# Kernel optimization log

Measured on AMD Instinct MI355X. Metric: run time of the kernel, lower is better.

Reference implementation:

```python
import jax, jax.numpy as jnp
import numpy as np

N = 100000        # nodes
E = 1600000       # edges
D = 32            # hidden dim
C = 2             # num classes
NL = 4            # layer_num - 1 GIN layers
G = 512           # graphs in batch
BN_EPS = 1e-3     # keras BatchNormalization default epsilon


def setup_inputs() -> dict:
    key = jax.random.key(0)
    ks = jax.random.split(key, 16)
    s = 0.1
    return {
        "node_embeddings": jax.random.normal(ks[0], (N, D), dtype=jnp.float32),
        "edge_index": jax.random.randint(ks[1], (2, E), 0, N, dtype=jnp.int32),
        "batch": jnp.sort(jax.random.randint(ks[2], (N,), 0, G, dtype=jnp.int32)),
        # MLP inner dense + BN (per GIN layer)
        "W1": jax.random.normal(ks[3], (NL, D, D), dtype=jnp.float32) * s,
        "b1": jnp.zeros((NL, D), jnp.float32),
        "bn1_g": jnp.ones((NL, D), jnp.float32),
        "bn1_b": jnp.zeros((NL, D), jnp.float32),
        # MLP output dense
        "W2": jax.random.normal(ks[4], (NL, D, D), dtype=jnp.float32) * s,
        "b2": jnp.zeros((NL, D), jnp.float32),
        # ApplyNodeFunc BN
        "bn2_g": jnp.ones((NL, D), jnp.float32),
        "bn2_b": jnp.zeros((NL, D), jnp.float32),
        # outer per-layer BN
        "norm_g": jnp.ones((NL, D), jnp.float32),
        "norm_b": jnp.zeros((NL, D), jnp.float32),
        # readout heads: one Dense(num_classes) per hidden_rep level (layer_num of them)
        "dense_W": jax.random.normal(ks[5], (NL + 1, D, C), dtype=jnp.float32) * s,
        "dense_b": jnp.zeros((NL + 1, C), jnp.float32),
    }


def _bn(x, g, b):
    # inference-mode BatchNorm with init moving stats (mean=0, var=1)
    return x * (g / jnp.sqrt(1.0 + BN_EPS)) + b


def reference(node_embeddings, edge_index, batch, W1, b1, bn1_g, bn1_b,
              W2, b2, bn2_g, bn2_b, norm_g, norm_b, dense_W, dense_b):
    src, dst = edge_index[0], edge_index[1]
    h = node_embeddings
    hidden = [h]
    for i in range(NL):
        # GIN aggregation: (1+eps)*h + sum of neighbor features (eps=0)
        agg = jax.ops.segment_sum(h[src], dst, num_segments=N)  # [N, D]
        z = h + agg
        # ApplyNodeFunc: MLP (Dense->BN->ReLU->Dense) then BN + ReLU
        z = jax.nn.relu(_bn(z @ W1[i] + b1[i], bn1_g[i], bn1_b[i]))
        z = z @ W2[i] + b2[i]
        z = jax.nn.relu(_bn(z, bn2_g[i], bn2_b[i]))
        # outer norm + relu
        h = jax.nn.relu(_bn(z, norm_g[i], norm_b[i]))
        hidden.append(h)
    # readout: segment-sum pooling per hidden level, Dense(num_classes), summed
    score = jnp.zeros((G, C), dtype=node_embeddings.dtype)
    for i, hr in enumerate(hidden):
        pool = jax.ops.segment_sum(hr, batch, num_segments=G)  # [G, D]
        score = score + pool @ dense_W[i] + dense_b[i]
    return jax.nn.softmax(score, axis=-1)
```

## Files before the change

### kernel.cpp

```cpp
#include <hip/hip_runtime.h>

#define NN 100000
#define EE 1600000
#define DD 32
#define CC 2
#define NLAYERS 4
#define GG 512

#define BSH 9
#define BW 512
#define NBUK ((NN + BW - 1) / BW)
#define CAP 12288
#define CH 2048
#define NPART ((EE + CH - 1) / CH)

__global__ void part_kernel(const int* __restrict__ ei,
                            int* __restrict__ gcur,
                            unsigned* __restrict__ part) {
    __shared__ unsigned sorted[CH];
    __shared__ unsigned char sbkt[CH];
    __shared__ int cnt[NBUK], offs[NBUK], cur[NBUK], gbs[NBUK];

    const int tid = threadIdx.x;
    const int eb  = blockIdx.x * CH;
    const int nch = min(CH, EE - eb);

    for (int b = tid; b < NBUK; b += 256) cnt[b] = 0;
    __syncthreads();
    for (int i = tid; i < nch; i += 256) {
        int dn = ei[EE + eb + i];
        atomicAdd(&cnt[dn >> BSH], 1);
    }
    __syncthreads();
    if (tid == 0) {
        int o = 0;
        for (int b = 0; b < NBUK; ++b) { offs[b] = o; o += cnt[b]; }
    }
    __syncthreads();
    if (tid < NBUK) {
        cur[tid] = offs[tid];
        gbs[tid] = cnt[tid] ? atomicAdd(&gcur[tid], cnt[tid]) : 0;
    }
    __syncthreads();
    for (int i = tid; i < nch; i += 256) {
        int s  = ei[eb + i];
        int dn = ei[EE + eb + i];
        int b  = dn >> BSH;
        unsigned pk = ((unsigned)(dn & (BW - 1)) << 17) | (unsigned)s;
        int p = atomicAdd(&cur[b], 1);
        sorted[p] = pk;
        sbkt[p]   = (unsigned char)b;
    }
    __syncthreads();
    for (int i = tid; i < nch; i += 256) {
        int b = sbkt[i];
        part[(size_t)b * CAP + gbs[b] + (i - offs[b])] = sorted[i];
    }
}

__global__ void bscan_kernel(const int* __restrict__ gcur,
                             int* __restrict__ bbase,
                             int* __restrict__ row_ptr) {
    if (threadIdx.x == 0 && blockIdx.x == 0) {
        int o = 0;
        for (int b = 0; b < NBUK; ++b) { bbase[b] = o; o += gcur[b]; }
        row_ptr[NN] = EE;
    }
}

__global__ void lcsr_kernel(const unsigned* __restrict__ part,
                            const int* __restrict__ gcur,
                            const int* __restrict__ bbase,
                            int* __restrict__ row_ptr,
                            unsigned* __restrict__ csr_packed) {
    __shared__ int hcnt[BW];
    __shared__ int a[2][BW];
    __shared__ int ccur[BW];
    const int t    = threadIdx.x;
    const int b    = blockIdx.x;
    const int cntb = gcur[b];
    const int base = bbase[b];
    const size_t pb = (size_t)b * CAP;

    hcnt[t] = 0;
    __syncthreads();
    for (int i = t; i < cntb; i += BW)
        atomicAdd(&hcnt[part[pb + i] >> 17], 1);
    __syncthreads();
    int x = hcnt[t];
    a[0][t] = x;
    __syncthreads();
    int cb = 0;
    for (int off = 1; off < BW; off <<= 1) {
        int v = a[cb][t];
        if (t >= off) v += a[cb][t - off];
        a[cb ^ 1][t] = v;
        cb ^= 1;
        __syncthreads();
    }
    const int excl = a[cb][t] - x;
    const int node = b * BW + t;
    if (node < NN) row_ptr[node] = base + excl;
    ccur[t] = excl;
    __syncthreads();
    for (int i = t; i < cntb; i += BW) {
        unsigned pk = part[pb + i];
        int dl  = pk >> 17;
        int pos = base + atomicAdd(&ccur[dl], 1);
        csr_packed[pos] = ((unsigned)(dl & 63) << 17) | (pk & 0x1FFFFu);
    }
}

__global__ __launch_bounds__(256) void layer_kernel(
    const float* __restrict__ h_in, float* __restrict__ h_out,
    const int* __restrict__ row_ptr, const unsigned* __restrict__ csr_packed,
    const int* __restrict__ batch,
    const float* __restrict__ W1, const float* __restrict__ b1,
    const float* __restrict__ g1, const float* __restrict__ bt1,
    const float* __restrict__ W2, const float* __restrict__ b2,
    const float* __restrict__ g2, const float* __restrict__ bt2,
    const float* __restrict__ ng, const float* __restrict__ nb,
    const float* __restrict__ dWl, float* __restrict__ score) {
    __shared__ float sp[8 * DD];
    __shared__ float sdW[DD * CC];
    __shared__ float ss[GG * CC];
    __shared__ float zA[64][DD];
    __shared__ float z2loc[8][DD];

    const int tid = threadIdx.x;
    const int j = tid >> 5;
    const int d = tid & 31;

    if (tid < DD) {
        sp[0 * DD + tid] = b1[tid];
        sp[1 * DD + tid] = g1[tid];
        sp[2 * DD + tid] = bt1[tid];
        sp[3 * DD + tid] = b2[tid];
        sp[4 * DD + tid] = g2[tid];
        sp[5 * DD + tid] = bt2[tid];
        sp[6 * DD + tid] = ng[tid];
        sp[7 * DD + tid] = nb[tid];
    }
    if (tid < DD * CC) sdW[tid] = dWl[tid];
    for (int i = tid; i < GG * CC; i += 256) ss[i] = 0.f;

    const float invs = 1.0f / sqrtf(1.001f);
    const int base = blockIdx.x * 64;

    for (int s = 0; s < 8; ++s) {
        const int local = j * 8 + s;
        const int n = base + local;
        if (n >= NN) break;
        float acc = h_in[(size_t)n * DD + d];
        int e = row_ptr[n];
        const int e1 = row_ptr[n + 1];
        for (; e + 16 <= e1; e += 16) {
            unsigned ix[16];
            #pragma unroll
            for (int i = 0; i < 16; ++i) ix[i] = csr_packed[e + i] & 0x1FFFFu;
            float v[16];
            #pragma unroll
            for (int i = 0; i < 16; ++i) v[i] = h_in[(size_t)ix[i] * DD + d];
            float t0 = ((v[0] + v[1]) + (v[2] + v[3])) +
                       ((v[4] + v[5]) + (v[6] + v[7]));
            float t1 = ((v[8] + v[9]) + (v[10] + v[11])) +
                       ((v[12] + v[13]) + (v[14] + v[15]));
            acc += t0 + t1;
        }
        if (e + 8 <= e1) {
            unsigned ix[8];
            #pragma unroll
            for (int i = 0; i < 8; ++i) ix[i] = csr_packed[e + i] & 0x1FFFFu;
            float v[8];
            #pragma unroll
            for (int i = 0; i < 8; ++i) v[i] = h_in[(size_t)ix[i] * DD + d];
            acc += ((v[0] + v[1]) + (v[2] + v[3])) +
                   ((v[4] + v[5]) + (v[6] + v[7]));
            e += 8;
        }
        if (e + 4 <= e1) {
            unsigned ix[4];
            #pragma unroll
            for (int i = 0; i < 4; ++i) ix[i] = csr_packed[e + i] & 0x1FFFFu;
            float v[4];
            #pragma unroll
            for (int i = 0; i < 4; ++i) v[i] = h_in[(size_t)ix[i] * DD + d];
            acc += (v[0] + v[1]) + (v[2] + v[3]);
            e += 4;
        }
        for (; e < e1; ++e)
            acc += h_in[(size_t)(csr_packed[e] & 0x1FFFFu) * DD + d];
        zA[local][d] = acc;
    }
    __syncthreads();

    for (int s = 0; s < 8; ++s) {
        const int local = j * 8 + s;
        const int n = base + local;
        if (n >= NN) break;

        float a1 = sp[0 * DD + d];
        #pragma unroll
        for (int kk = 0; kk < DD; kk += 4) {
            const float4 zv = *reinterpret_cast<const float4*>(&zA[local][kk]);
            a1 += zv.x * W1[(kk + 0) * DD + d] + zv.y * W1[(kk + 1) * DD + d] +
                  zv.z * W1[(kk + 2) * DD + d] + zv.w * W1[(kk + 3) * DD + d];
        }
        float v = fmaxf(a1 * (sp[1 * DD + d] * invs) + sp[2 * DD + d], 0.f);
        z2loc[j][d] = v;

        float a2 = sp[3 * DD + d];
        #pragma unroll
        for (int kk = 0; kk < DD; kk += 4) {
            const float4 zv = *reinterpret_cast<const float4*>(&z2loc[j][kk]);
            a2 += zv.x * W2[(kk + 0) * DD + d] + zv.y * W2[(kk + 1) * DD + d] +
                  zv.z * W2[(kk + 2) * DD + d] + zv.w * W2[(kk + 3) * DD + d];
        }
        float w = fmaxf(a2 * (sp[4 * DD + d] * invs) + sp[5 * DD + d], 0.f);
        w = fmaxf(w * (sp[6 * DD + d] * invs) + sp[7 * DD + d], 0.f);
        h_out[(size_t)n * DD + d] = w;

        float p0 = w * sdW[d * CC + 0];
        float p1 = w * sdW[d * CC + 1];
        #pragma unroll
        for (int off = 16; off > 0; off >>= 1) {
            p0 += __shfl_xor(p0, off, 32);
            p1 += __shfl_xor(p1, off, 32);
        }
        if (d == 0) {
            int g = batch[n];
            atomicAdd(&ss[g * CC + 0], p0);
            atomicAdd(&ss[g * CC + 1], p1);
        }
    }
    __syncthreads();

    for (int i = tid; i < GG * CC; i += 256) {
        float v = ss[i];
        if (v != 0.f) atomicAdd(&score[i], v);
    }
}

__global__ void pool_kernel(const float* __restrict__ h,
                            const int* __restrict__ batch,
                            const float* __restrict__ Wd,
                            float* __restrict__ score) {
    __shared__ float ss[GG * CC];
    __shared__ float sW[DD * CC];
    const int tid = threadIdx.x;
    for (int i = tid; i < GG * CC; i += 256) ss[i] = 0.f;
    if (tid < DD * CC) sW[tid] = Wd[tid];
    __syncthreads();

    const int d = tid & 31;
    const int grp = tid >> 5;
    const int n0 = blockIdx.x * 512;
    const int n1 = (n0 + 512 < NN) ? (n0 + 512) : NN;

    for (int n = n0 + grp; n < n1; n += 8) {
        float v = h[(size_t)n * DD + d];
        float p0 = v * sW[d * CC + 0];
        float p1 = v * sW[d * CC + 1];
        #pragma unroll
        for (int off = 16; off > 0; off >>= 1) {
            p0 += __shfl_xor(p0, off, 32);
            p1 += __shfl_xor(p1, off, 32);
        }
        if (d == 0) {
            int g = batch[n];
            atomicAdd(&ss[g * CC + 0], p0);
            atomicAdd(&ss[g * CC + 1], p1);
        }
    }
    __syncthreads();

    for (int i = tid; i < GG * CC; i += 256) {
        float v = ss[i];
        if (v != 0.f) atomicAdd(&score[i], v);
    }
}

__global__ void softmax_kernel(const float* __restrict__ score,
                               const float* __restrict__ db,
                               float* __restrict__ out) {
    int g = blockIdx.x * blockDim.x + threadIdx.x;
    if (g >= GG) return;
    float bs0 = 0.f, bs1 = 0.f;
    #pragma unroll
    for (int i = 0; i <= NLAYERS; ++i) {
        bs0 += db[i * CC + 0];
        bs1 += db[i * CC + 1];
    }
    float s0 = score[g * CC + 0] + bs0;
    float s1 = score[g * CC + 1] + bs1;
    float m = fmaxf(s0, s1);
    float e0 = expf(s0 - m), e1 = expf(s1 - m);
    float inv = 1.f / (e0 + e1);
    out[g * CC + 0] = e0 * inv;
    out[g * CC + 1] = e1 * inv;
}

extern "C" void kernel_launch(void* const* d_in, const int* in_sizes, int n_in,
                              void* d_out, int out_size, void* d_ws, size_t ws_size,
                              hipStream_t stream) {
    (void)in_sizes; (void)n_in; (void)out_size; (void)ws_size;

    const float* node_emb = (const float*)d_in[0];
    const int*   ei       = (const int*)d_in[1];
    const int*   batch    = (const int*)d_in[2];
    const float* W1       = (const float*)d_in[3];
    const float* b1       = (const float*)d_in[4];
    const float* g1       = (const float*)d_in[5];
    const float* bt1      = (const float*)d_in[6];
    const float* W2       = (const float*)d_in[7];
    const float* b2       = (const float*)d_in[8];
    const float* g2       = (const float*)d_in[9];
    const float* bt2      = (const float*)d_in[10];
    const float* ng       = (const float*)d_in[11];
    const float* nb       = (const float*)d_in[12];
    const float* dW       = (const float*)d_in[13];
    const float* db       = (const float*)d_in[14];
    float* out = (float*)d_out;

    float* hA      = (float*)d_ws;
    float* hB      = hA + (size_t)NN * DD;
    unsigned* part = (unsigned*)hB;
    float* score   = hB + (size_t)NN * DD;
    int* row_ptr   = (int*)(score + GG * CC);
    unsigned* csr_packed = (unsigned*)(row_ptr + NN + 2);
    int* gcur      = (int*)(csr_packed + EE);
    int* bbase     = gcur + 256;

    hipMemsetAsync(gcur, 0, 256 * sizeof(int), stream);
    hipMemsetAsync(score, 0, GG * CC * sizeof(float), stream);

    part_kernel<<<NPART, 256, 0, stream>>>(ei, gcur, part);
    bscan_kernel<<<1, 64, 0, stream>>>(gcur, bbase, row_ptr);
    lcsr_kernel<<<NBUK, BW, 0, stream>>>(part, gcur, bbase, row_ptr, csr_packed);

    pool_kernel<<<(NN + 511) / 512, 256, 0, stream>>>(node_emb, batch, dW, score);

    const int layerGrid = (NN + 63) / 64;
    const float* cur_in = node_emb;
    float* bufs[2] = {hA, hB};
    for (int i = 0; i < NLAYERS; ++i) {
        float* o = bufs[i & 1];
        layer_kernel<<<layerGrid, 256, 0, stream>>>(
            cur_in, o, row_ptr, csr_packed, batch,
            W1 + (size_t)i * DD * DD, b1 + i * DD, g1 + i * DD, bt1 + i * DD,
            W2 + (size_t)i * DD * DD, b2 + i * DD, g2 + i * DD, bt2 + i * DD,
            ng + i * DD, nb + i * DD,
            dW + (size_t)(i + 1) * DD * CC, score);
        cur_in = o;
    }

    softmax_kernel<<<(GG + 255) / 256, 256, 0, stream>>>(score, db, out);
}
```

Before: 443.5 us.

## Shrink layer blocks, drop shared score buffer, and run-length accumulate graph atomics

Each layer block now handles 32 nodes instead of 64 (4 per warp), giving more blocks and less shared memory per block. The 512-graph shared score array, its zeroing and its final flush loop are removed. Since nodes are sorted by graph, each warp instead keeps a run-length accumulator and issues global atomics only when the graph id changes. BN parameters live in registers instead of shared memory, CSR stores plain source ids without masking, and the bounds checks go away because NN divides evenly by 32. The risk is more global atomic traffic on the score array.

```diff
diff --git a/kernel.cpp b/kernel.cpp
--- a/kernel.cpp
+++ b/kernel.cpp
@@ -13,6 +13,9 @@
 #define CAP 12288
 #define CH 2048
 #define NPART ((EE + CH - 1) / CH)
+
+#define NPB 32
+#define NPG 4
 
 __global__ void part_kernel(const int* __restrict__ ei,
                             int* __restrict__ gcur,
@@ -72,7 +75,7 @@
                             const int* __restrict__ gcur,
                             const int* __restrict__ bbase,
                             int* __restrict__ row_ptr,
-                            unsigned* __restrict__ csr_packed) {
+                            int* __restrict__ csr_src) {
     __shared__ int hcnt[BW];
     __shared__ int a[2][BW];
     __shared__ int ccur[BW];
@@ -107,13 +110,13 @@
         unsigned pk = part[pb + i];
         int dl  = pk >> 17;
         int pos = base + atomicAdd(&ccur[dl], 1);
-        csr_packed[pos] = ((unsigned)(dl & 63) << 17) | (pk & 0x1FFFFu);
+        csr_src[pos] = (int)(pk & 0x1FFFFu);
     }
 }
 
 __global__ __launch_bounds__(256) void layer_kernel(
     const float* __restrict__ h_in, float* __restrict__ h_out,
-    const int* __restrict__ row_ptr, const unsigned* __restrict__ csr_packed,
+    const int* __restrict__ row_ptr, const int* __restrict__ csr_src,
     const int* __restrict__ batch,
     const float* __restrict__ W1, const float* __restrict__ b1,
     const float* __restrict__ g1, const float* __restrict__ bt1,
@@ -121,43 +124,38 @@
     const float* __restrict__ g2, const float* __restrict__ bt2,
     const float* __restrict__ ng, const float* __restrict__ nb,
     const float* __restrict__ dWl, float* __restrict__ score) {
-    __shared__ float sp[8 * DD];
-    __shared__ float sdW[DD * CC];
-    __shared__ float ss[GG * CC];
-    __shared__ float zA[64][DD];
+    __shared__ float zA[NPB][DD];
     __shared__ float z2loc[8][DD];
 
     const int tid = threadIdx.x;
     const int j = tid >> 5;
     const int d = tid & 31;
 
-    if (tid < DD) {
-        sp[0 * DD + tid] = b1[tid];
-        sp[1 * DD + tid] = g1[tid];
-        sp[2 * DD + tid] = bt1[tid];
-        sp[3 * DD + tid] = b2[tid];
-        sp[4 * DD + tid] = g2[tid];
-        sp[5 * DD + tid] = bt2[tid];
-        sp[6 * DD + tid] = ng[tid];
-        sp[7 * DD + tid] = nb[tid];
-    }
-    if (tid < DD * CC) sdW[tid] = dWl[tid];
-    for (int i = tid; i < GG * CC; i += 256) ss[i] = 0.f;
-
     const float invs = 1.0f / sqrtf(1.001f);
-    const int base = blockIdx.x * 64;
-
-    for (int s = 0; s < 8; ++s) {
-        const int local = j * 8 + s;
+    const float B1v = b1[d];
+    const float G1v = g1[d] * invs;
+    const float T1v = bt1[d];
+    const float B2v = b2[d];
+    const float G2v = g2[d] * invs;
+    const float T2v = bt2[d];
+    const float Gnv = ng[d] * invs;
+    const float Tnv = nb[d];
+    const float Wd0 = dWl[d * CC + 0];
+    const float Wd1 = dWl[d * CC + 1];
+
+    const int base = blockIdx.x * NPB;
+
+    #pragma unroll
+    for (int s = 0; s < NPG; ++s) {
+        const int local = j * NPG + s;
         const int n = base + local;
-        if (n >= NN) break;
         float acc = h_in[(size_t)n * DD + d];
         int e = row_ptr[n];
         const int e1 = row_ptr[n + 1];
         for (; e + 16 <= e1; e += 16) {
-            unsigned ix[16];
-            #pragma unroll
-            for (int i = 0; i < 16; ++i) ix[i] = csr_packed[e + i] & 0x1FFFFu;
+            int ix[16];
+            #pragma unroll
+            for (int i = 0; i < 16; ++i) ix[i] = csr_src[e + i];
             float v[16];
             #pragma unroll
             for (int i = 0; i < 16; ++i) v[i] = h_in[(size_t)ix[i] * DD + d];
@@ -168,9 +166,9 @@
             acc += t0 + t1;
         }
         if (e + 8 <= e1) {
-            unsigned ix[8];
-            #pragma unroll
-            for (int i = 0; i < 8; ++i) ix[i] = csr_packed[e + i] & 0x1FFFFu;
+            int ix[8];
+            #pragma unroll
+            for (int i = 0; i < 8; ++i) ix[i] = csr_src[e + i];
             float v[8];
             #pragma unroll
             for (int i = 0; i < 8; ++i) v[i] = h_in[(size_t)ix[i] * DD + d];
@@ -179,9 +177,9 @@
             e += 8;
         }
         if (e + 4 <= e1) {
-            unsigned ix[4];
-            #pragma unroll
-            for (int i = 0; i < 4; ++i) ix[i] = csr_packed[e + i] & 0x1FFFFu;
+            int ix[4];
+            #pragma unroll
+            for (int i = 0; i < 4; ++i) ix[i] = csr_src[e + i];
             float v[4];
             #pragma unroll
             for (int i = 0; i < 4; ++i) v[i] = h_in[(size_t)ix[i] * DD + d];
@@ -189,39 +187,40 @@
             e += 4;
         }
         for (; e < e1; ++e)
-            acc += h_in[(size_t)(csr_packed[e] & 0x1FFFFu) * DD + d];
+            acc += h_in[(size_t)csr_src[e] * DD + d];
         zA[local][d] = acc;
     }
-    __syncthreads();
-
-    for (int s = 0; s < 8; ++s) {
-        const int local = j * 8 + s;
+
+    int   curg = -1;
+    float a0 = 0.f, a1s = 0.f;
+    #pragma unroll
+    for (int s = 0; s < NPG; ++s) {
+        const int local = j * NPG + s;
         const int n = base + local;
-        if (n >= NN) break;
-
-        float a1 = sp[0 * DD + d];
+
+        float m1 = B1v;
         #pragma unroll
         for (int kk = 0; kk < DD; kk += 4) {
             const float4 zv = *reinterpret_cast<const float4*>(&zA[local][kk]);
-            a1 += zv.x * W1[(kk + 0) * DD + d] + zv.y * W1[(kk + 1) * DD + d] +
+            m1 += zv.x * W1[(kk + 0) * DD + d] + zv.y * W1[(kk + 1) * DD + d] +
                   zv.z * W1[(kk + 2) * DD + d] + zv.w * W1[(kk + 3) * DD + d];
         }
-        float v = fmaxf(a1 * (sp[1 * DD + d] * invs) + sp[2 * DD + d], 0.f);
+        float v = fmaxf(m1 * G1v + T1v, 0.f);
         z2loc[j][d] = v;
 
-        float a2 = sp[3 * DD + d];
+        float m2 = B2v;
         #pragma unroll
         for (int kk = 0; kk < DD; kk += 4) {
             const float4 zv = *reinterpret_cast<const float4*>(&z2loc[j][kk]);
-            a2 += zv.x * W2[(kk + 0) * DD + d] + zv.y * W2[(kk + 1) * DD + d] +
+            m2 += zv.x * W2[(kk + 0) * DD + d] + zv.y * W2[(kk + 1) * DD + d] +
                   zv.z * W2[(kk + 2) * DD + d] + zv.w * W2[(kk + 3) * DD + d];
         }
-        float w = fmaxf(a2 * (sp[4 * DD + d] * invs) + sp[5 * DD + d], 0.f);
-        w = fmaxf(w * (sp[6 * DD + d] * invs) + sp[7 * DD + d], 0.f);
+        float w = fmaxf(m2 * G2v + T2v, 0.f);
+        w = fmaxf(w * Gnv + Tnv, 0.f);
         h_out[(size_t)n * DD + d] = w;
 
-        float p0 = w * sdW[d * CC + 0];
-        float p1 = w * sdW[d * CC + 1];
+        float p0 = w * Wd0;
+        float p1 = w * Wd1;
         #pragma unroll
         for (int off = 16; off > 0; off >>= 1) {
             p0 += __shfl_xor(p0, off, 32);
@@ -229,15 +228,19 @@
         }
         if (d == 0) {
             int g = batch[n];
-            atomicAdd(&ss[g * CC + 0], p0);
-            atomicAdd(&ss[g * CC + 1], p1);
-        }
-    }
-    __syncthreads();
-
-    for (int i = tid; i < GG * CC; i += 256) {
-        float v = ss[i];
-        if (v != 0.f) atomicAdd(&score[i], v);
+            if (g != curg) {
+                if (curg >= 0) {
+                    atomicAdd(&score[curg * CC + 0], a0);
+                    atomicAdd(&score[curg * CC + 1], a1s);
+                }
+                curg = g; a0 = 0.f; a1s = 0.f;
+            }
+            a0 += p0; a1s += p1;
+        }
+    }
+    if (d == 0 && curg >= 0) {
+        atomicAdd(&score[curg * CC + 0], a0);
+        atomicAdd(&score[curg * CC + 1], a1s);
     }
 }
 
@@ -327,8 +330,8 @@
     unsigned* part = (unsigned*)hB;
     float* score   = hB + (size_t)NN * DD;
     int* row_ptr   = (int*)(score + GG * CC);
-    unsigned* csr_packed = (unsigned*)(row_ptr + NN + 2);
-    int* gcur      = (int*)(csr_packed + EE);
+    int* csr_src   = row_ptr + NN + 2;
+    int* gcur      = csr_src + EE;
     int* bbase     = gcur + 256;
 
     hipMemsetAsync(gcur, 0, 256 * sizeof(int), stream);
@@ -336,17 +339,17 @@
 
     part_kernel<<<NPART, 256, 0, stream>>>(ei, gcur, part);
     bscan_kernel<<<1, 64, 0, stream>>>(gcur, bbase, row_ptr);
-    lcsr_kernel<<<NBUK, BW, 0, stream>>>(part, gcur, bbase, row_ptr, csr_packed);
+    lcsr_kernel<<<NBUK, BW, 0, stream>>>(part, gcur, bbase, row_ptr, csr_src);
 
     pool_kernel<<<(NN + 511) / 512, 256, 0, stream>>>(node_emb, batch, dW, score);
 
-    const int layerGrid = (NN + 63) / 64;
+    const int layerGrid = NN / NPB;
     const float* cur_in = node_emb;
     float* bufs[2] = {hA, hB};
     for (int i = 0; i < NLAYERS; ++i) {
         float* o = bufs[i & 1];
         layer_kernel<<<layerGrid, 256, 0, stream>>>(
-            cur_in, o, row_ptr, csr_packed, batch,
+            cur_in, o, row_ptr, csr_src, batch,
             W1 + (size_t)i * DD * DD, b1 + i * DD, g1 + i * DD, bt1 + i * DD,
             W2 + (size_t)i * DD * DD, b2 + i * DD, g2 + i * DD, bt2 + i * DD,
             ng + i * DD, nb + i * DD,
```

New measurement: 525.7 us. 1.19x slower.
